# Performance work log

Hardware: AMD Instinct MI355X
Metric: run time of the kernel (lower is better)

Reference implementation:

```python
import jax, jax.numpy as jnp
import numpy as np

S, N, I, H = 512, 64, 256, 1024
T = 128


def setup_inputs() -> dict:
    key = jax.random.key(0)
    ks = jax.random.split(key, 16)
    sc = 0.05
    inp = {
        "x": jax.random.normal(ks[0], (S, N, I), dtype=jnp.float32),
        "target_len": T,
        # encoder LSTM params (torch gate order i,f,g,o stacked along 4H)
        "We_ih": jax.random.normal(ks[1], (4 * H, I), dtype=jnp.float32) * sc,
        "We_hh": jax.random.normal(ks[2], (4 * H, H), dtype=jnp.float32) * sc,
        "be": jax.random.normal(ks[3], (4 * H,), dtype=jnp.float32) * sc,
        # decoder LSTM params
        "Wd_ih": jax.random.normal(ks[4], (4 * H, I), dtype=jnp.float32) * sc,
        "Wd_hh": jax.random.normal(ks[5], (4 * H, H), dtype=jnp.float32) * sc,
        "bd": jax.random.normal(ks[6], (4 * H,), dtype=jnp.float32) * sc,
        # attention: linear1, linear2 (H->I), linear3 (I->1)
        "W1": jax.random.normal(ks[7], (I, H), dtype=jnp.float32) * sc,
        "b1": jax.random.normal(ks[8], (I,), dtype=jnp.float32) * sc,
        "W2": jax.random.normal(ks[9], (I, H), dtype=jnp.float32) * sc,
        "b2": jax.random.normal(ks[10], (I,), dtype=jnp.float32) * sc,
        "w3": jax.random.normal(ks[11], (I,), dtype=jnp.float32) * sc,
        "b3": jax.random.normal(ks[12], (), dtype=jnp.float32) * sc,
        # decoder output linear (H->I)
        "Wl": jax.random.normal(ks[13], (I, H), dtype=jnp.float32) * sc,
        "bl": jax.random.normal(ks[14], (I,), dtype=jnp.float32) * sc,
    }
    return inp


def _lstm_gates(pre, h, W_hh):
    # pre: (N,4H) = x@W_ih^T + b ; torch gate order i,f,g,o
    g = pre + h @ W_hh.T
    i, f, gg, o = jnp.split(g, 4, axis=-1)
    return jax.nn.sigmoid(i), jax.nn.sigmoid(f), jnp.tanh(gg), jax.nn.sigmoid(o)


def reference(x, target_len, We_ih, We_hh, be, Wd_ih, Wd_hh, bd,
              W1, b1, W2, b2, w3, b3, Wl, bl):
    n = x.shape[1]
    # ---- Encoder: full-sequence LSTM, zero initial state ----
    xp = jnp.einsum('sni,gi->sng', x, We_ih) + be  # (S,N,4H)

    def enc_step(carry, pre_t):
        h, c = carry
        i, f, g, o = _lstm_gates(pre_t, h, We_hh)
        c_new = f * c + i * g
        h_new = o * jnp.tanh(c_new)
        return (h_new, c_new), h_new

    h0 = jnp.zeros((n, H), dtype=x.dtype)
    (h_e, c_e), out_e = jax.lax.scan(enc_step, (h0, h0), xp)  # out_e: (S,N,H)

    # precompute linear2(out_e) once (shared across decode steps)
    pre2 = jnp.einsum('snh,ih->sni', out_e, W2) + b2  # (S,N,I)

    # ---- Decoder loop with Bahdanau attention ----
    def dec_step(carry, _):
        input_d, h_d, c_d = carry  # (N,I), (N,H), (N,H)
        # attention scores over source positions (softmax along S)
        e = jnp.tanh(pre2 + h_d @ W1.T + b1)           # (S,N,I)
        scores = e @ w3 + b3                            # (S,N)
        alpha = jax.nn.softmax(scores, axis=0)          # (S,N)
        ctx = jnp.einsum('sn,snh->nh', alpha, out_e)    # (N,H) -> new hidden_d
        # single decoder LSTM step with hidden=ctx, cell=c_d
        pre = input_d @ Wd_ih.T + bd
        i, f, g, o = _lstm_gates(pre, ctx, Wd_hh)
        c_new = f * c_d + i * g
        h_new = o * jnp.tanh(c_new)
        out_d = h_new @ Wl.T + bl                       # (N,I)
        return (out_d, h_new, c_new), out_d

    init = (x[-1], h_e, c_e)
    _, outputs = jax.lax.scan(dec_step, init, None, length=target_len)
    return outputs  # (target_len, N, I)
```

## Files before the change

kernel.cpp:

```cpp
#include <hip/hip_runtime.h>

constexpr int Sx = 512;
constexpr int Nb = 64;
constexpr int Iw = 256;
constexpr int Hd = 1024;
constexpr int Td = 128;
constexpr int NH = Nb * Hd;
constexpr int NI = Nb * Iw;
constexpr int NBLK = 256;
constexpr int NTHR = 512;

#define DEVFN __device__ __forceinline__

DEVFN float sigmoidf_(float x) { return 1.0f / (1.0f + __expf(-x)); }
DEVFN float tanhf_(float x) {
  const float t = __expf(-2.0f * fabsf(x));
  const float r = (1.0f - t) / (1.0f + t);
  return copysignf(r, x);
}

DEVFN void gridbar(int* cnt, int* gen) {
  __syncthreads();
  if (threadIdx.x == 0) {
    __threadfence();
    int g = __hip_atomic_load(gen, __ATOMIC_RELAXED, __HIP_MEMORY_SCOPE_AGENT);
    int a = __hip_atomic_fetch_add(cnt, 1, __ATOMIC_ACQ_REL, __HIP_MEMORY_SCOPE_AGENT);
    if (a == NBLK - 1) {
      __hip_atomic_store(cnt, 0, __ATOMIC_RELAXED, __HIP_MEMORY_SCOPE_AGENT);
      __hip_atomic_fetch_add(gen, 1, __ATOMIC_RELEASE, __HIP_MEMORY_SCOPE_AGENT);
    } else {
      while (__hip_atomic_load(gen, __ATOMIC_RELAXED, __HIP_MEMORY_SCOPE_AGENT) == g)
        __builtin_amdgcn_s_sleep(2);
    }
    __threadfence();
  }
  __syncthreads();
}

DEVFN void lstm_tile_step(
    const float* hsrc,
    const float* xsrc,
    float* hdst,
    const float* w_lds, float* stage, float* c_lds, const float* b_lds,
    int j0, int tid)
{
  const int rg = tid >> 7;
  const int ng = (tid >> 3) & 15;
  const int ks = tid & 7;
  float acc[4][4];
  #pragma unroll
  for (int i = 0; i < 4; ++i)
    #pragma unroll
    for (int j = 0; j < 4; ++j) acc[i][j] = 0.f;

  for (int c = 0; c < 5; ++c) {
    __syncthreads();
    const float* src = (c < 4) ? (hsrc + c * 256) : xsrc;
    const int sstr = (c < 4) ? Hd : Iw;
    for (int idx = tid; idx < 4096; idx += NTHR) {
      const int nn = idx >> 6, kf = idx & 63;
      const float4 v = *(const float4*)(src + (size_t)nn * sstr + kf * 4);
      float* d = stage + nn * 258 + kf * 4;
      d[0] = v.x; d[1] = v.y; d[2] = v.z; d[3] = v.w;
    }
    __syncthreads();
    #pragma unroll
    for (int kk = 0; kk < 8; ++kk) {
      const int kf4 = kk * 8 + ks;
      float4 wv[4];
      #pragma unroll
      for (int i = 0; i < 4; ++i)
        wv[i] = *(const float4*)(w_lds + (size_t)(rg * 4 + i) * 1280 + c * 256 + kf4 * 4);
      #pragma unroll
      for (int j = 0; j < 4; ++j) {
        const float* hp = stage + (ng * 4 + j) * 258 + kf4 * 4;
        const float h0 = hp[0], h1 = hp[1], h2 = hp[2], h3 = hp[3];
        #pragma unroll
        for (int i = 0; i < 4; ++i) {
          acc[i][j] = fmaf(wv[i].x, h0, acc[i][j]);
          acc[i][j] = fmaf(wv[i].y, h1, acc[i][j]);
          acc[i][j] = fmaf(wv[i].z, h2, acc[i][j]);
          acc[i][j] = fmaf(wv[i].w, h3, acc[i][j]);
        }
      }
    }
  }
  __syncthreads();
  #pragma unroll
  for (int i = 0; i < 4; ++i)
    #pragma unroll
    for (int j = 0; j < 4; ++j)
      stage[((rg * 4 + i) * 64 + (ng * 4 + j)) * 8 + ks] = acc[i][j];
  __syncthreads();
  if (tid < 256) {
    const int n = tid >> 2, jj = tid & 3;
    float v[4];
    #pragma unroll
    for (int g = 0; g < 4; ++g) {
      const int r = g * 4 + jj;
      const float* p = stage + ((size_t)r * 64 + n) * 8;
      v[g] = b_lds[r] + ((p[0] + p[1]) + (p[2] + p[3])) + ((p[4] + p[5]) + (p[6] + p[7]));
    }
    const float ig = sigmoidf_(v[0]);
    const float fg = sigmoidf_(v[1]);
    const float gg = tanhf_(v[2]);
    const float og = sigmoidf_(v[3]);
    const float cn = fg * c_lds[tid] + ig * gg;
    c_lds[tid] = cn;
    hdst[(size_t)n * Hd + j0 + jj] = og * tanhf_(cn);
  }
}

__global__ __launch_bounds__(NTHR, 2) void enc_mega(
    const float* __restrict__ x, const float* __restrict__ We_ih,
    const float* __restrict__ We_hh, const float* __restrict__ be,
    const float* __restrict__ zero_h, float* out_e, float* c_glob,
    int* barcnt, int* bargen)
{
  __shared__ float w_lds[16 * 1280];
  __shared__ float stage[64 * 258];
  __shared__ float c_lds[256];
  __shared__ float b_lds[16];
  const int tid = threadIdx.x;
  const int j0 = blockIdx.x * 4;

  for (int r = 0; r < 16; ++r) {
    const int grow = (r >> 2) * Hd + j0 + (r & 3);
    const float4* sh = (const float4*)(We_hh + (size_t)grow * Hd);
    for (int kf = tid; kf < 256; kf += NTHR)
      *(float4*)(w_lds + (size_t)r * 1280 + kf * 4) = sh[kf];
    const float4* si = (const float4*)(We_ih + (size_t)grow * Iw);
    for (int kf = tid; kf < 64; kf += NTHR)
      *(float4*)(w_lds + (size_t)r * 1280 + 1024 + kf * 4) = si[kf];
  }
  if (tid < 16) b_lds[tid] = be[(tid >> 2) * Hd + j0 + (tid & 3)];
  if (tid < 256) c_lds[tid] = 0.f;

  for (int t = 0; t < Sx; ++t) {
    const float* hprev = t ? (out_e + (size_t)(t - 1) * NH) : zero_h;
    lstm_tile_step(hprev, x + (size_t)t * NI, out_e + (size_t)t * NH,
                   w_lds, stage, c_lds, b_lds, j0, tid);
    gridbar(barcnt, bargen);
  }
  if (tid < 256) {
    const int n = tid >> 2, jj = tid & 3;
    c_glob[(size_t)n * Hd + j0 + jj] = c_lds[tid];
  }
}

__global__ __launch_bounds__(256) void pre2_kernel(
    const float* __restrict__ oute, const float* __restrict__ W2,
    const float* __restrict__ b2, float* __restrict__ pre2)
{
  __shared__ float hl[16 * 1024];
  const int tid = threadIdx.x;
  const int sn0 = blockIdx.x * 16;
  {
    const float4* src = (const float4*)(oute + (size_t)sn0 * Hd);
    float4* dst = (float4*)hl;
    for (int idx = tid; idx < 4096; idx += 256) dst[idx] = src[idx];
  }
  __syncthreads();
  const int i = tid;
  const float4* __restrict__ w = (const float4*)(W2 + (size_t)i * Hd);
  float acc[16];
  #pragma unroll
  for (int ss = 0; ss < 16; ++ss) acc[ss] = 0.0f;
  #pragma unroll 2
  for (int k4 = 0; k4 < 256; ++k4) {
    const float4 wv = w[k4];
    #pragma unroll
    for (int ss = 0; ss < 16; ++ss) {
      const float4 hv = *(const float4*)(hl + ss * 1024 + k4 * 4);
      acc[ss] = fmaf(wv.x, hv.x, acc[ss]); acc[ss] = fmaf(wv.y, hv.y, acc[ss]);
      acc[ss] = fmaf(wv.z, hv.z, acc[ss]); acc[ss] = fmaf(wv.w, hv.w, acc[ss]);
    }
  }
  const float bb = b2[i];
  #pragma unroll
  for (int ss = 0; ss < 16; ++ss)
    pre2[(size_t)(sn0 + ss) * Iw + i] = acc[ss] + bb;
}

__global__ __launch_bounds__(NTHR, 2) void dec_mega(
    const float* __restrict__ x, const float* __restrict__ Wd_ih,
    const float* __restrict__ Wd_hh, const float* __restrict__ bd,
    const float* __restrict__ W1, const float* __restrict__ b1,
    const float* __restrict__ w3, const float* __restrict__ b3,
    const float* __restrict__ Wl, const float* __restrict__ bl,
    const float* out_e, const float* __restrict__ pre2,
    const float* __restrict__ c_glob,
    float* q, float* scores, float* ctx, float* h_d, float* out,
    int* barcnt, int* bargen)
{
  __shared__ float w_lds[16 * 1280];
  __shared__ float stage[64 * 258];
  __shared__ float c_lds[256];
  __shared__ float b_lds[16];
  __shared__ float aux[512];
  const int tid = threadIdx.x;
  const int b = blockIdx.x;
  const int j0 = b * 4;

  for (int r = 0; r < 16; ++r) {
    const int grow = (r >> 2) * Hd + j0 + (r & 3);
    const float4* sh = (const float4*)(Wd_hh + (size_t)grow * Hd);
    for (int kf = tid; kf < 256; kf += NTHR)
      *(float4*)(w_lds + (size_t)r * 1280 + kf * 4) = sh[kf];
    const float4* si = (const float4*)(Wd_ih + (size_t)grow * Iw);
    for (int kf = tid; kf < 64; kf += NTHR)
      *(float4*)(w_lds + (size_t)r * 1280 + 1024 + kf * 4) = si[kf];
  }
  if (tid < 16) b_lds[tid] = bd[(tid >> 2) * Hd + j0 + (tid & 3)];
  if (tid < 256) {
    const int n = tid >> 2, jj = tid & 3;
    c_lds[tid] = c_glob[(size_t)n * Hd + j0 + jj];
  }

  const int role = b >> 7;
  const int i0 = (b & 127) * 2;

  for (int t = 0; t <= Td; ++t) {
    const float* hin = t ? h_d : (out_e + (size_t)(Sx - 1) * NH);
    {
      const bool active = (role == 0) ? (t < Td) : (t > 0);
      if (active) {
        const float* W = role ? Wl : W1;
        const float* bias = role ? bl : b1;
        float* dst = role ? (out + (size_t)(t - 1) * NI) : q;
        const int nn = tid >> 3, ks = tid & 7;
        float a0 = 0.f, a1 = 0.f;
        const float4* hr = (const float4*)(hin + (size_t)nn * Hd);
        const float4* w0 = (const float4*)(W + (size_t)i0 * Hd);
        const float4* w1 = (const float4*)(W + (size_t)(i0 + 1) * Hd);
        #pragma unroll 4
        for (int kk = 0; kk < 32; ++kk) {
          const int kf4 = kk * 8 + ks;
          const float4 hv = hr[kf4];
          const float4 v0 = w0[kf4], v1 = w1[kf4];
          a0 = fmaf(hv.x, v0.x, a0); a0 = fmaf(hv.y, v0.y, a0);
          a0 = fmaf(hv.z, v0.z, a0); a0 = fmaf(hv.w, v0.w, a0);
          a1 = fmaf(hv.x, v1.x, a1); a1 = fmaf(hv.y, v1.y, a1);
          a1 = fmaf(hv.z, v1.z, a1); a1 = fmaf(hv.w, v1.w, a1);
        }
        __syncthreads();
        stage[(nn * 2 + 0) * 8 + ks] = a0;
        stage[(nn * 2 + 1) * 8 + ks] = a1;
        __syncthreads();
        if (tid < 128) {
          const int n = tid >> 1, ii = tid & 1;
          const float* p = stage + (n * 2 + ii) * 8;
          const float s = ((p[0] + p[1]) + (p[2] + p[3])) + ((p[4] + p[5]) + (p[6] + p[7]));
          dst[(size_t)n * Iw + i0 + ii] = s + bias[i0 + ii];
        }
      }
    }
    if (t == Td) break;
    gridbar(barcnt, bargen);

    {
      const int sn = tid >> 2, isl = tid & 3;
      const int s = 2 * b + (sn >> 6);
      const int n = sn & 63;
      const float* pr = pre2 + ((size_t)s * Nb + n) * Iw + isl * 64;
      const float* qr = q + (size_t)n * Iw + isl * 64;
      const float* wr = w3 + isl * 64;
      float a = 0.f;
      #pragma unroll 4
      for (int m = 0; m < 16; ++m) {
        const float4 p = *(const float4*)(pr + m * 4);
        const float4 qv = *(const float4*)(qr + m * 4);
        const float4 wv = *(const float4*)(wr + m * 4);
        a += tanhf_(p.x + qv.x) * wv.x + tanhf_(p.y + qv.y) * wv.y
           + tanhf_(p.z + qv.z) * wv.z + tanhf_(p.w + qv.w) * wv.w;
      }
      __syncthreads();
      aux[tid] = a;
      __syncthreads();
      if (tid < 128) {
        const int s2 = 2 * b + (tid >> 6);
        const int n2 = tid & 63;
        const float* p = aux + tid * 4;
        scores[(size_t)n2 * Sx + s2] = (p[0] + p[1]) + (p[2] + p[3]) + b3[0];
      }
    }
    gridbar(barcnt, bargen);

    {
      const int n = b >> 2, hq = b & 3;
      const float sv = scores[(size_t)n * Sx + tid];
      __syncthreads();
      aux[tid] = sv;
      __syncthreads();
      for (int w = 256; w >= 1; w >>= 1) {
        if (tid < w) aux[tid] = fmaxf(aux[tid], aux[tid + w]);
        __syncthreads();
      }
      const float mx = aux[0];
      __syncthreads();
      const float ev = __expf(sv - mx);
      aux[tid] = ev;
      __syncthreads();
      for (int w = 256; w >= 1; w >>= 1) {
        if (tid < w) aux[tid] += aux[tid + w];
        __syncthreads();
      }
      const float inv = 1.0f / aux[0];
      __syncthreads();
      stage[tid] = ev * inv;
      __syncthreads();
      const int h4 = tid & 63, ss = tid >> 6;
      const float* base = out_e + (size_t)n * Hd + hq * 256 + h4 * 4;
      float A0 = 0.f, A1 = 0.f, A2 = 0.f, A3 = 0.f;
      for (int si = ss * 64; si < ss * 64 + 64; ++si) {
        const float al = stage[si];
        const float4 v = *(const float4*)(base + (size_t)si * NH);
        A0 = fmaf(al, v.x, A0); A1 = fmaf(al, v.y, A1);
        A2 = fmaf(al, v.z, A2); A3 = fmaf(al, v.w, A3);
      }
      stage[512 + (h4 * 4 + 0) * 8 + ss] = A0;
      stage[512 + (h4 * 4 + 1) * 8 + ss] = A1;
      stage[512 + (h4 * 4 + 2) * 8 + ss] = A2;
      stage[512 + (h4 * 4 + 3) * 8 + ss] = A3;
      __syncthreads();
      if (tid < 256) {
        const float* p = stage + 512 + (size_t)tid * 8;
        const float v = ((p[0] + p[1]) + (p[2] + p[3])) + ((p[4] + p[5]) + (p[6] + p[7]));
        ctx[(size_t)n * Hd + hq * 256 + tid] = v;
      }
    }
    gridbar(barcnt, bargen);

    {
      const float* inp = t ? (out + (size_t)(t - 1) * NI) : (x + (size_t)(Sx - 1) * NI);
      lstm_tile_step(ctx, inp, h_d, w_lds, stage, c_lds, b_lds, j0, tid);
    }
    gridbar(barcnt, bargen);
  }
}

extern "C" void kernel_launch(void* const* d_in, const int* in_sizes, int n_in,
                              void* d_out, int out_size, void* d_ws, size_t ws_size,
                              hipStream_t stream) {
  (void)in_sizes; (void)n_in; (void)out_size; (void)ws_size;
  const float* x     = (const float*)d_in[0];
  const float* We_ih = (const float*)d_in[2];
  const float* We_hh = (const float*)d_in[3];
  const float* be    = (const float*)d_in[4];
  const float* Wd_ih = (const float*)d_in[5];
  const float* Wd_hh = (const float*)d_in[6];
  const float* bd    = (const float*)d_in[7];
  const float* W1    = (const float*)d_in[8];
  const float* b1    = (const float*)d_in[9];
  const float* W2    = (const float*)d_in[10];
  const float* b2    = (const float*)d_in[11];
  const float* w3    = (const float*)d_in[12];
  const float* b3    = (const float*)d_in[13];
  const float* Wl    = (const float*)d_in[14];
  const float* bl    = (const float*)d_in[15];
  float* out = (float*)d_out;

  float* ws     = (float*)d_ws;
  float* out_e  = ws;
  float* pre2   = out_e + (size_t)Sx * NH;
  float* zero_h = pre2 + (size_t)Sx * NI;
  float* c_glob = zero_h + NH;
  float* qb     = c_glob + NH;
  float* scb    = qb + NI;
  float* ctxb   = scb + Nb * Sx;
  float* h_d    = ctxb + NH;
  int*   bar    = (int*)(h_d + NH);

  hipMemsetAsync(zero_h, 0, (size_t)NH * sizeof(float), stream);
  hipMemsetAsync(bar, 0, 128 * sizeof(int), stream);

  int* barcnt = bar;
  int* bargen = bar + 64;

  {
    void* args[] = {(void*)&x, (void*)&We_ih, (void*)&We_hh, (void*)&be,
                    (void*)&zero_h, (void*)&out_e, (void*)&c_glob,
                    (void*)&barcnt, (void*)&bargen};
    hipLaunchCooperativeKernel(reinterpret_cast<void*>(enc_mega),
                               dim3(NBLK), dim3(NTHR), args, 0, stream);
  }

  pre2_kernel<<<2048, 256, 0, stream>>>(out_e, W2, b2, pre2);

  {
    void* args[] = {(void*)&x, (void*)&Wd_ih, (void*)&Wd_hh, (void*)&bd,
                    (void*)&W1, (void*)&b1, (void*)&w3, (void*)&b3,
                    (void*)&Wl, (void*)&bl, (void*)&out_e, (void*)&pre2,
                    (void*)&c_glob, (void*)&qb, (void*)&scb, (void*)&ctxb,
                    (void*)&h_d, (void*)&out, (void*)&barcnt, (void*)&bargen};
    hipLaunchCooperativeKernel(reinterpret_cast<void*>(dec_mega),
                               dim3(NBLK), dim3(NTHR), args, 0, stream);
  }
}
```

Baseline: 39.36 ms.

## Store encoder outputs and pre2 in bf16, retile LSTM matvec, ping-pong hidden state

The encoder now writes its hidden sequence as bf16 and keeps fp32 h in two ping-pong buffers. pre2 is computed and stored in bf16, and the decoder's attention scoring and context reduction read the bf16 data and widen it in registers. The LSTM tile matvec is reorganised to 8x8 register tiles with a wave-shuffle partial reduction and padded LDS strides, and one redundant sync is dropped. The aim is to halve the memory traffic of the attention passes over the 512-step sequence and to raise FMA density per LDS load, at the cost of bf16 rounding error in the attention inputs.

```diff
diff --git a/kernel.cpp b/kernel.cpp
--- a/kernel.cpp
+++ b/kernel.cpp
@@ -1,4 +1,7 @@
 #include <hip/hip_runtime.h>
+
+typedef unsigned short ushort_t;
+typedef unsigned int uint_t;
 
 constexpr int Sx = 512;
 constexpr int Nb = 64;
@@ -9,6 +12,8 @@
 constexpr int NI = Nb * Iw;
 constexpr int NBLK = 256;
 constexpr int NTHR = 512;
+constexpr int WROW = 1284;
+constexpr int SROW = 260;
 
 #define DEVFN __device__ __forceinline__
 
@@ -17,6 +22,13 @@
   const float t = __expf(-2.0f * fabsf(x));
   const float r = (1.0f - t) / (1.0f + t);
   return copysignf(r, x);
+}
+DEVFN float bflo(uint_t u) { return __uint_as_float(u << 16); }
+DEVFN float bfhi(uint_t u) { return __uint_as_float(u & 0xFFFF0000u); }
+DEVFN ushort_t f2b(float f) {
+  uint_t u = __float_as_uint(f);
+  u = (u + 0x7FFFu + ((u >> 16) & 1u)) >> 16;
+  return (ushort_t)u;
 }
 
 DEVFN void gridbar(int* cnt, int* gen) {
@@ -41,65 +53,81 @@
     const float* hsrc,
     const float* xsrc,
     float* hdst,
+    ushort_t* hdst_b16,
     const float* w_lds, float* stage, float* c_lds, const float* b_lds,
     int j0, int tid)
 {
-  const int rg = tid >> 7;
-  const int ng = (tid >> 3) & 15;
-  const int ks = tid & 7;
-  float acc[4][4];
+  const int np = tid & 7;
+  const int rp = (tid >> 3) & 1;
+  const int ks = tid >> 4;
+
+  float acc[8][8];
   #pragma unroll
-  for (int i = 0; i < 4; ++i)
-    #pragma unroll
-    for (int j = 0; j < 4; ++j) acc[i][j] = 0.f;
+  for (int i = 0; i < 8; ++i)
+    #pragma unroll
+    for (int j = 0; j < 8; ++j) acc[i][j] = 0.f;
 
   for (int c = 0; c < 5; ++c) {
     __syncthreads();
     const float* src = (c < 4) ? (hsrc + c * 256) : xsrc;
     const int sstr = (c < 4) ? Hd : Iw;
     for (int idx = tid; idx < 4096; idx += NTHR) {
-      const int nn = idx >> 6, kf = idx & 63;
-      const float4 v = *(const float4*)(src + (size_t)nn * sstr + kf * 4);
-      float* d = stage + nn * 258 + kf * 4;
-      d[0] = v.x; d[1] = v.y; d[2] = v.z; d[3] = v.w;
+      const int kq = idx & 63, nn = idx >> 6;
+      *(float4*)(stage + nn * SROW + kq * 4) =
+          *(const float4*)(src + (size_t)nn * sstr + kq * 4);
     }
     __syncthreads();
     #pragma unroll
-    for (int kk = 0; kk < 8; ++kk) {
-      const int kf4 = kk * 8 + ks;
-      float4 wv[4];
+    for (int kk = 0; kk < 2; ++kk) {
+      const int kq = kk * 32 + ks;
+      const int wq = c * 64 + kq;
+      float4 wv[8];
       #pragma unroll
-      for (int i = 0; i < 4; ++i)
-        wv[i] = *(const float4*)(w_lds + (size_t)(rg * 4 + i) * 1280 + c * 256 + kf4 * 4);
+      for (int j = 0; j < 8; ++j)
+        wv[j] = *(const float4*)(w_lds + (size_t)(rp * 8 + j) * WROW + wq * 4);
       #pragma unroll
-      for (int j = 0; j < 4; ++j) {
-        const float* hp = stage + (ng * 4 + j) * 258 + kf4 * 4;
-        const float h0 = hp[0], h1 = hp[1], h2 = hp[2], h3 = hp[3];
+      for (int i = 0; i < 8; ++i) {
+        const float4 hq = *(const float4*)(stage + (size_t)(i * 8 + np) * SROW + kq * 4);
         #pragma unroll
-        for (int i = 0; i < 4; ++i) {
-          acc[i][j] = fmaf(wv[i].x, h0, acc[i][j]);
-          acc[i][j] = fmaf(wv[i].y, h1, acc[i][j]);
-          acc[i][j] = fmaf(wv[i].z, h2, acc[i][j]);
-          acc[i][j] = fmaf(wv[i].w, h3, acc[i][j]);
+        for (int j = 0; j < 8; ++j) {
+          acc[i][j] = fmaf(hq.x, wv[j].x, acc[i][j]);
+          acc[i][j] = fmaf(hq.y, wv[j].y, acc[i][j]);
+          acc[i][j] = fmaf(hq.z, wv[j].z, acc[i][j]);
+          acc[i][j] = fmaf(hq.w, wv[j].w, acc[i][j]);
         }
       }
     }
   }
+
+  #pragma unroll
+  for (int i = 0; i < 8; ++i)
+    #pragma unroll
+    for (int j = 0; j < 8; ++j) {
+      float v = acc[i][j];
+      v += __shfl_xor(v, 16);
+      v += __shfl_xor(v, 32);
+      acc[i][j] = v;
+    }
   __syncthreads();
-  #pragma unroll
-  for (int i = 0; i < 4; ++i)
-    #pragma unroll
-    for (int j = 0; j < 4; ++j)
-      stage[((rg * 4 + i) * 64 + (ng * 4 + j)) * 8 + ks] = acc[i][j];
+  const int wv8 = tid >> 6;
+  if ((tid & 48) == 0) {
+    #pragma unroll
+    for (int i = 0; i < 8; ++i)
+      #pragma unroll
+      for (int j = 0; j < 8; ++j) {
+        const int r = rp * 8 + j, n = i * 8 + np;
+        stage[(size_t)(r * 64 + n) * 9 + wv8] = acc[i][j];
+      }
+  }
   __syncthreads();
   if (tid < 256) {
     const int n = tid >> 2, jj = tid & 3;
     float v[4];
     #pragma unroll
     for (int g = 0; g < 4; ++g) {
-      const int r = g * 4 + jj;
-      const float* p = stage + ((size_t)r * 64 + n) * 8;
-      v[g] = b_lds[r] + ((p[0] + p[1]) + (p[2] + p[3])) + ((p[4] + p[5]) + (p[6] + p[7]));
+      const float* p = stage + (size_t)((g * 4 + jj) * 64 + n) * 9;
+      float s = ((p[0] + p[1]) + (p[2] + p[3])) + ((p[4] + p[5]) + (p[6] + p[7]));
+      v[g] = b_lds[g * 4 + jj] + s;
     }
     const float ig = sigmoidf_(v[0]);
     const float fg = sigmoidf_(v[1]);
@@ -107,38 +135,46 @@
     const float og = sigmoidf_(v[3]);
     const float cn = fg * c_lds[tid] + ig * gg;
     c_lds[tid] = cn;
-    hdst[(size_t)n * Hd + j0 + jj] = og * tanhf_(cn);
-  }
+    const float hv = og * tanhf_(cn);
+    hdst[(size_t)n * Hd + j0 + jj] = hv;
+    if (hdst_b16) hdst_b16[(size_t)n * Hd + j0 + jj] = f2b(hv);
+  }
+}
+
+DEVFN void load_weights(const float* Whh, const float* Wih, const float* bias,
+                        float* w_lds, float* b_lds, int j0, int tid) {
+  for (int r = 0; r < 16; ++r) {
+    const int grow = (r >> 2) * Hd + j0 + (r & 3);
+    const float4* sh = (const float4*)(Whh + (size_t)grow * Hd);
+    for (int kf = tid; kf < 256; kf += NTHR)
+      *(float4*)(w_lds + (size_t)r * WROW + kf * 4) = sh[kf];
+    const float4* si = (const float4*)(Wih + (size_t)grow * Iw);
+    for (int kf = tid; kf < 64; kf += NTHR)
+      *(float4*)(w_lds + (size_t)r * WROW + 1024 + kf * 4) = si[kf];
+  }
+  if (tid < 16) b_lds[tid] = bias[(tid >> 2) * Hd + j0 + (tid & 3)];
 }
 
 __global__ __launch_bounds__(NTHR, 2) void enc_mega(
     const float* __restrict__ x, const float* __restrict__ We_ih,
     const float* __restrict__ We_hh, const float* __restrict__ be,
-    const float* __restrict__ zero_h, float* out_e, float* c_glob,
+    float* hbuf0, float* hbuf1, ushort_t* out_eb, float* c_glob,
     int* barcnt, int* bargen)
 {
-  __shared__ float w_lds[16 * 1280];
-  __shared__ float stage[64 * 258];
+  __shared__ float w_lds[16 * WROW];
+  __shared__ float stage[64 * SROW];
   __shared__ float c_lds[256];
   __shared__ float b_lds[16];
   const int tid = threadIdx.x;
   const int j0 = blockIdx.x * 4;
 
-  for (int r = 0; r < 16; ++r) {
-    const int grow = (r >> 2) * Hd + j0 + (r & 3);
-    const float4* sh = (const float4*)(We_hh + (size_t)grow * Hd);
-    for (int kf = tid; kf < 256; kf += NTHR)
-      *(float4*)(w_lds + (size_t)r * 1280 + kf * 4) = sh[kf];
-    const float4* si = (const float4*)(We_ih + (size_t)grow * Iw);
-    for (int kf = tid; kf < 64; kf += NTHR)
-      *(float4*)(w_lds + (size_t)r * 1280 + 1024 + kf * 4) = si[kf];
-  }
-  if (tid < 16) b_lds[tid] = be[(tid >> 2) * Hd + j0 + (tid & 3)];
+  load_weights(We_hh, We_ih, be, w_lds, b_lds, j0, tid);
   if (tid < 256) c_lds[tid] = 0.f;
 
   for (int t = 0; t < Sx; ++t) {
-    const float* hprev = t ? (out_e + (size_t)(t - 1) * NH) : zero_h;
-    lstm_tile_step(hprev, x + (size_t)t * NI, out_e + (size_t)t * NH,
+    float* hin = (t & 1) ? hbuf1 : hbuf0;
+    float* hout = (t & 1) ? hbuf0 : hbuf1;
+    lstm_tile_step(hin, x + (size_t)t * NI, hout, out_eb + (size_t)t * NH,
                    w_lds, stage, c_lds, b_lds, j0, tid);
     gridbar(barcnt, bargen);
   }
@@ -149,16 +185,18 @@
 }
 
 __global__ __launch_bounds__(256) void pre2_kernel(
-    const float* __restrict__ oute, const float* __restrict__ W2,
-    const float* __restrict__ b2, float* __restrict__ pre2)
+    const ushort_t* __restrict__ outeb, const float* __restrict__ W2,
+    const float* __restrict__ b2, ushort_t* __restrict__ pre2b)
 {
   __shared__ float hl[16 * 1024];
   const int tid = threadIdx.x;
   const int sn0 = blockIdx.x * 16;
-  {
-    const float4* src = (const float4*)(oute + (size_t)sn0 * Hd);
-    float4* dst = (float4*)hl;
-    for (int idx = tid; idx < 4096; idx += 256) dst[idx] = src[idx];
+  for (int idx = tid; idx < 2048; idx += 256) {
+    const uint4 u = *(const uint4*)(outeb + (size_t)sn0 * Hd + idx * 8);
+    float4 a = {bflo(u.x), bfhi(u.x), bflo(u.y), bfhi(u.y)};
+    float4 b = {bflo(u.z), bfhi(u.z), bflo(u.w), bfhi(u.w)};
+    *(float4*)(hl + idx * 8) = a;
+    *(float4*)(hl + idx * 8 + 4) = b;
   }
   __syncthreads();
   const int i = tid;
@@ -179,7 +217,7 @@
   const float bb = b2[i];
   #pragma unroll
   for (int ss = 0; ss < 16; ++ss)
-    pre2[(size_t)(sn0 + ss) * Iw + i] = acc[ss] + bb;
+    pre2b[(size_t)(sn0 + ss) * Iw + i] = f2b(acc[ss] + bb);
 }
 
 __global__ __launch_bounds__(NTHR, 2) void dec_mega(
@@ -188,13 +226,13 @@
     const float* __restrict__ W1, const float* __restrict__ b1,
     const float* __restrict__ w3, const float* __restrict__ b3,
     const float* __restrict__ Wl, const float* __restrict__ bl,
-    const float* out_e, const float* __restrict__ pre2,
+    const float* h_e, const ushort_t* out_eb, const ushort_t* __restrict__ pre2b,
     const float* __restrict__ c_glob,
     float* q, float* scores, float* ctx, float* h_d, float* out,
     int* barcnt, int* bargen)
 {
-  __shared__ float w_lds[16 * 1280];
-  __shared__ float stage[64 * 258];
+  __shared__ float w_lds[16 * WROW];
+  __shared__ float stage[64 * SROW];
   __shared__ float c_lds[256];
   __shared__ float b_lds[16];
   __shared__ float aux[512];
@@ -202,16 +240,7 @@
   const int b = blockIdx.x;
   const int j0 = b * 4;
 
-  for (int r = 0; r < 16; ++r) {
-    const int grow = (r >> 2) * Hd + j0 + (r & 3);
-    const float4* sh = (const float4*)(Wd_hh + (size_t)grow * Hd);
-    for (int kf = tid; kf < 256; kf += NTHR)
-      *(float4*)(w_lds + (size_t)r * 1280 + kf * 4) = sh[kf];
-    const float4* si = (const float4*)(Wd_ih + (size_t)grow * Iw);
-    for (int kf = tid; kf < 64; kf += NTHR)
-      *(float4*)(w_lds + (size_t)r * 1280 + 1024 + kf * 4) = si[kf];
-  }
-  if (tid < 16) b_lds[tid] = bd[(tid >> 2) * Hd + j0 + (tid & 3)];
+  load_weights(Wd_hh, Wd_ih, bd, w_lds, b_lds, j0, tid);
   if (tid < 256) {
     const int n = tid >> 2, jj = tid & 3;
     c_lds[tid] = c_glob[(size_t)n * Hd + j0 + jj];
@@ -221,21 +250,21 @@
   const int i0 = (b & 127) * 2;
 
   for (int t = 0; t <= Td; ++t) {
-    const float* hin = t ? h_d : (out_e + (size_t)(Sx - 1) * NH);
+    const float* hin = t ? h_d : h_e;
     {
       const bool active = (role == 0) ? (t < Td) : (t > 0);
       if (active) {
         const float* W = role ? Wl : W1;
         const float* bias = role ? bl : b1;
         float* dst = role ? (out + (size_t)(t - 1) * NI) : q;
-        const int nn = tid >> 3, ks = tid & 7;
+        const int nn = tid >> 3, ksl = tid & 7;
         float a0 = 0.f, a1 = 0.f;
         const float4* hr = (const float4*)(hin + (size_t)nn * Hd);
         const float4* w0 = (const float4*)(W + (size_t)i0 * Hd);
         const float4* w1 = (const float4*)(W + (size_t)(i0 + 1) * Hd);
         #pragma unroll 4
         for (int kk = 0; kk < 32; ++kk) {
-          const int kf4 = kk * 8 + ks;
+          const int kf4 = kk * 8 + ksl;
           const float4 hv = hr[kf4];
           const float4 v0 = w0[kf4], v1 = w1[kf4];
           a0 = fmaf(hv.x, v0.x, a0); a0 = fmaf(hv.y, v0.y, a0);
@@ -244,8 +273,8 @@
           a1 = fmaf(hv.z, v1.z, a1); a1 = fmaf(hv.w, v1.w, a1);
         }
         __syncthreads();
-        stage[(nn * 2 + 0) * 8 + ks] = a0;
-        stage[(nn * 2 + 1) * 8 + ks] = a1;
+        stage[(nn * 2 + 0) * 8 + ksl] = a0;
+        stage[(nn * 2 + 1) * 8 + ksl] = a1;
         __syncthreads();
         if (tid < 128) {
           const int n = tid >> 1, ii = tid & 1;
@@ -262,17 +291,21 @@
       const int sn = tid >> 2, isl = tid & 3;
       const int s = 2 * b + (sn >> 6);
       const int n = sn & 63;
-      const float* pr = pre2 + ((size_t)s * Nb + n) * Iw + isl * 64;
+      const ushort_t* pr = pre2b + ((size_t)s * Nb + n) * Iw + isl * 64;
       const float* qr = q + (size_t)n * Iw + isl * 64;
       const float* wr = w3 + isl * 64;
       float a = 0.f;
-      #pragma unroll 4
-      for (int m = 0; m < 16; ++m) {
-        const float4 p = *(const float4*)(pr + m * 4);
-        const float4 qv = *(const float4*)(qr + m * 4);
-        const float4 wv = *(const float4*)(wr + m * 4);
-        a += tanhf_(p.x + qv.x) * wv.x + tanhf_(p.y + qv.y) * wv.y
-           + tanhf_(p.z + qv.z) * wv.z + tanhf_(p.w + qv.w) * wv.w;
+      #pragma unroll 2
+      for (int m = 0; m < 8; ++m) {
+        const uint4 u = *(const uint4*)(pr + m * 8);
+        const float4 q0 = *(const float4*)(qr + m * 8);
+        const float4 q1 = *(const float4*)(qr + m * 8 + 4);
+        const float4 w0 = *(const float4*)(wr + m * 8);
+        const float4 w1 = *(const float4*)(wr + m * 8 + 4);
+        a += tanhf_(bflo(u.x) + q0.x) * w0.x + tanhf_(bfhi(u.x) + q0.y) * w0.y
+           + tanhf_(bflo(u.y) + q0.z) * w0.z + tanhf_(bfhi(u.y) + q0.w) * w0.w;
+        a += tanhf_(bflo(u.z) + q1.x) * w1.x + tanhf_(bfhi(u.z) + q1.y) * w1.y
+           + tanhf_(bflo(u.w) + q1.z) * w1.z + tanhf_(bfhi(u.w) + q1.w) * w1.w;
       }
       __syncthreads();
       aux[tid] = a;
@@ -289,7 +322,6 @@
     {
       const int n = b >> 2, hq = b & 3;
       const float sv = scores[(size_t)n * Sx + tid];
-      __syncthreads();
       aux[tid] = sv;
       __syncthreads();
       for (int w = 256; w >= 1; w >>= 1) {
@@ -309,31 +341,37 @@
       __syncthreads();
       stage[tid] = ev * inv;
       __syncthreads();
-      const int h4 = tid & 63, ss = tid >> 6;
-      const float* base = out_e + (size_t)n * Hd + hq * 256 + h4 * 4;
-      float A0 = 0.f, A1 = 0.f, A2 = 0.f, A3 = 0.f;
-      for (int si = ss * 64; si < ss * 64 + 64; ++si) {
+      const int h8 = tid & 31, ss = tid >> 5;
+      const ushort_t* bp = out_eb + (size_t)n * Hd + hq * 256 + h8 * 8;
+      float A[8];
+      #pragma unroll
+      for (int e = 0; e < 8; ++e) A[e] = 0.f;
+      #pragma unroll 4
+      for (int si = ss * 32; si < ss * 32 + 32; ++si) {
         const float al = stage[si];
-        const float4 v = *(const float4*)(base + (size_t)si * NH);
-        A0 = fmaf(al, v.x, A0); A1 = fmaf(al, v.y, A1);
-        A2 = fmaf(al, v.z, A2); A3 = fmaf(al, v.w, A3);
-      }
-      stage[512 + (h4 * 4 + 0) * 8 + ss] = A0;
-      stage[512 + (h4 * 4 + 1) * 8 + ss] = A1;
-      stage[512 + (h4 * 4 + 2) * 8 + ss] = A2;
-      stage[512 + (h4 * 4 + 3) * 8 + ss] = A3;
+        const uint4 u = *(const uint4*)(bp + (size_t)si * NH);
+        A[0] = fmaf(al, bflo(u.x), A[0]); A[1] = fmaf(al, bfhi(u.x), A[1]);
+        A[2] = fmaf(al, bflo(u.y), A[2]); A[3] = fmaf(al, bfhi(u.y), A[3]);
+        A[4] = fmaf(al, bflo(u.z), A[4]); A[5] = fmaf(al, bfhi(u.z), A[5]);
+        A[6] = fmaf(al, bflo(u.w), A[6]); A[7] = fmaf(al, bfhi(u.w), A[7]);
+      }
+      float4 lo = {A[0], A[1], A[2], A[3]};
+      float4 hi = {A[4], A[5], A[6], A[7]};
+      *(float4*)(stage + 1024 + ss * 264 + h8 * 8) = lo;
+      *(float4*)(stage + 1024 + ss * 264 + h8 * 8 + 4) = hi;
       __syncthreads();
       if (tid < 256) {
-        const float* p = stage + 512 + (size_t)tid * 8;
-        const float v = ((p[0] + p[1]) + (p[2] + p[3])) + ((p[4] + p[5]) + (p[6] + p[7]));
-        ctx[(size_t)n * Hd + hq * 256 + tid] = v;
+        float s = 0.f;
+        #pragma unroll
+        for (int sg = 0; sg < 16; ++sg) s += stage[1024 + sg * 264 + tid];
+        ctx[(size_t)n * Hd + hq * 256 + tid] = s;
       }
     }
     gridbar(barcnt, bargen);
 
     {
       const float* inp = t ? (out + (size_t)(t - 1) * NI) : (x + (size_t)(Sx - 1) * NI);
-      lstm_tile_step(ctx, inp, h_d, w_lds, stage, c_lds, b_lds, j0, tid);
+      lstm_tile_step(ctx, inp, h_d, nullptr, w_lds, stage, c_lds, b_lds, j0, tid);
     }
     gridbar(barcnt, bargen);
   }
@@ -361,17 +399,18 @@
   float* out = (float*)d_out;
 
   float* ws     = (float*)d_ws;
-  float* out_e  = ws;
-  float* pre2   = out_e + (size_t)Sx * NH;
-  float* zero_h = pre2 + (size_t)Sx * NI;
-  float* c_glob = zero_h + NH;
+  float* hbuf0  = ws;
+  float* hbuf1  = hbuf0 + NH;
+  float* c_glob = hbuf1 + NH;
   float* qb     = c_glob + NH;
   float* scb    = qb + NI;
   float* ctxb   = scb + Nb * Sx;
   float* h_d    = ctxb + NH;
   int*   bar    = (int*)(h_d + NH);
-
-  hipMemsetAsync(zero_h, 0, (size_t)NH * sizeof(float), stream);
+  ushort_t* out_eb = (ushort_t*)(bar + 128);
+  ushort_t* pre2b  = out_eb + (size_t)Sx * NH;
+
+  hipMemsetAsync(hbuf0, 0, (size_t)NH * sizeof(float), stream);
   hipMemsetAsync(bar, 0, 128 * sizeof(int), stream);
 
   int* barcnt = bar;
@@ -379,20 +418,22 @@
 
   {
     void* args[] = {(void*)&x, (void*)&We_ih, (void*)&We_hh, (void*)&be,
-                    (void*)&zero_h, (void*)&out_e, (void*)&c_glob,
+                    (void*)&hbuf0, (void*)&hbuf1, (void*)&out_eb, (void*)&c_glob,
                     (void*)&barcnt, (void*)&bargen};
     hipLaunchCooperativeKernel(reinterpret_cast<void*>(enc_mega),
                                dim3(NBLK), dim3(NTHR), args, 0, stream);
   }
 
-  pre2_kernel<<<2048, 256, 0, stream>>>(out_e, W2, b2, pre2);
+  pre2_kernel<<<2048, 256, 0, stream>>>(out_eb, W2, b2, pre2b);
 
   {
+    float* h_e = hbuf0;
     void* args[] = {(void*)&x, (void*)&Wd_ih, (void*)&Wd_hh, (void*)&bd,
                     (void*)&W1, (void*)&b1, (void*)&w3, (void*)&b3,
-                    (void*)&Wl, (void*)&bl, (void*)&out_e, (void*)&pre2,
-                    (void*)&c_glob, (void*)&qb, (void*)&scb, (void*)&ctxb,
-                    (void*)&h_d, (void*)&out, (void*)&barcnt, (void*)&bargen};
+                    (void*)&Wl, (void*)&bl, (void*)&h_e, (void*)&out_eb,
+                    (void*)&pre2b, (void*)&c_glob, (void*)&qb, (void*)&scb,
+                    (void*)&ctxb, (void*)&h_d, (void*)&out,
+                    (void*)&barcnt, (void*)&bargen};
     hipLaunchCooperativeKernel(reinterpret_cast<void*>(dec_mega),
                                dim3(NBLK), dim3(NTHR), args, 0, stream);
   }
```

Result: no change. 38.62 ms (-1.9%).
